# Kernel tuning notes

Hardware: AMD Instinct MI355X
Metric: run time of the kernel (lower is better)

## Reference

```python
import jax, jax.numpy as jnp
import numpy as np

INPUT_DIM = 512
HIDDEN_DIM = 512
SEQ_LEN = 512
BATCH = 128


def setup_inputs() -> dict:
    key = jax.random.key(0)
    ks = jax.random.split(key, 9)
    d_in = INPUT_DIM + HIDDEN_DIM
    s = 1.0 / np.sqrt(d_in)  # torch nn.Linear default init scale
    def lin(k):
        kw, kb = jax.random.split(k)
        W = jax.random.uniform(kw, (d_in, HIDDEN_DIM), jnp.float32, -s, s)
        b = jax.random.uniform(kb, (HIDDEN_DIM,), jnp.float32, -s, s)
        return W, b
    Wf, bf = lin(ks[0])
    Wi, bi = lin(ks[1])
    Wg, bg = lin(ks[2])
    Wo, bo = lin(ks[3])
    inputs = jax.random.normal(ks[4], (SEQ_LEN, BATCH, INPUT_DIM), jnp.float32)
    return {"inputs": inputs, "Wf": Wf, "bf": bf, "Wi": Wi, "bi": bi,
            "Wg": Wg, "bg": bg, "Wo": Wo, "bo": bo}


def reference(inputs, Wf, bf, Wi, bi, Wg, bg, Wo, bo):
    # Classical LSTM recurrence (n_qubits=0 path). inputs: [T, B, D_in]
    B = inputs.shape[1]
    hx = jnp.zeros((B, HIDDEN_DIM), inputs.dtype)
    cx = jnp.zeros((B, HIDDEN_DIM), inputs.dtype)
    # Stack the 4 gate weights so each step does one fused GEMM: [B, 1024] x [1024, 4H]
    W = jnp.concatenate([Wf, Wi, Wg, Wo], axis=1)  # [D_in+H, 4H]
    b = jnp.concatenate([bf, bi, bg, bo], axis=0)  # [4H]

    def step(carry, x):
        hx, cx = carry
        combined = jnp.concatenate([x, hx], axis=1)      # [B, D_in+H]
        gates = combined @ W + b                          # [B, 4H]
        f_, i_, g_, o_ = jnp.split(gates, 4, axis=1)
        f = jax.nn.sigmoid(f_)
        i = jax.nn.sigmoid(i_)
        g = jnp.tanh(g_)
        o = jax.nn.sigmoid(o_)
        cx = f * cx + i * g
        hx = o * jnp.tanh(cx)
        return (hx, cx), hx

    (hx, cx), outputs = jax.lax.scan(step, (hx, cx), inputs)
    return outputs, (hx, cx)
```

## Files before the change

kernel.cpp:

```cpp
#include <hip/hip_runtime.h>


typedef unsigned short u16;
typedef unsigned int   u32;
typedef unsigned long long u64;
typedef short bf16x8 __attribute__((ext_vector_type(8)));
typedef float f32x4  __attribute__((ext_vector_type(4)));

#define TT 512
#define BB 128
#define DD 512
#define HH 512
#define ASTRIDE 1032

__device__ __forceinline__ float bf2f(u16 u) { return __uint_as_float(((u32)u) << 16); }
__device__ __forceinline__ u16 f2bf(float f) {
    u32 u = __float_as_uint(f);
    return (u16)((u + 0x7FFFu + ((u >> 16) & 1u)) >> 16);
}
__device__ __forceinline__ u32 pack2(u16 a, u16 b) { return (u32)a | ((u32)b << 16); }
__device__ __forceinline__ float sigm(float x)  { return 1.0f / (1.0f + __expf(-x)); }
__device__ __forceinline__ float tanh_(float x) { return 1.0f - 2.0f / (1.0f + __expf(2.0f * x)); }

__launch_bounds__(256, 1)
__global__ void lstm_fused(const float* __restrict__ x,
                           const float* __restrict__ Wf, const float* __restrict__ bfv,
                           const float* __restrict__ Wi, const float* __restrict__ biv,
                           const float* __restrict__ Wg, const float* __restrict__ bgv,
                           const float* __restrict__ Wo, const float* __restrict__ bov,
                           float* __restrict__ out, u32* __restrict__ cnt,
                           u32* __restrict__ hbuf)
{
    __shared__ __align__(16) u16   aHi[16 * ASTRIDE];
    __shared__ __align__(16) u16   aLo[16 * ASTRIDE];
    __shared__ __align__(16) float xchg[4 * 4 * 16 * 20];

    const int tid  = threadIdx.x;
    const int lane = tid & 63;
    const int wv   = tid >> 6;
    const int l16  = lane & 15;
    const int quad = lane >> 4;
    const int blk  = blockIdx.x;
    const int mg   = blk & 7;
    const int nb   = blk >> 3;
    const int rowbase = mg * 16;
    const int kwb  = wv * 256;

    const float* Wq[4] = { Wf, Wi, Wg, Wo };
    bf16x8 whi[4][8], wlo[4][8];
#pragma unroll
    for (int q = 0; q < 4; ++q) {
        const float* Wp = Wq[q] + (size_t)(kwb + quad * 8) * HH + nb * 16 + l16;
#pragma unroll
        for (int s = 0; s < 8; ++s)
#pragma unroll
            for (int j = 0; j < 8; ++j) {
                float wval = Wp[(size_t)(s * 32 + j) * HH];
                u16 h = f2bf(wval);
                whi[q][s][j] = (short)h;
                wlo[q][s][j] = (short)f2bf(wval - bf2f(h));
            }
    }

    const int ec = tid & 15, er = tid >> 4;
    const int hcol = nb * 16 + ec;
    const float bias[4] = { bfv[hcol], biv[hcol], bgv[hcol], bov[hcol] };
    float cst = 0.0f;

    u32* myCnt = cnt + mg * 32;
    const int frow = tid >> 4;
    const int fch  = tid & 15;
    const u16* aHiB = aHi + l16 * ASTRIDE + kwb + quad * 8;
    const u16* aLoB = aLo + l16 * ASTRIDE + kwb + quad * 8;

    for (int t = 0; t < TT; ++t) {
        {
            u16* rowHi = aHi + frow * ASTRIDE;
            u16* rowLo = aLo + frow * ASTRIDE;
            const float4* xs = (const float4*)(x + ((size_t)t * BB + rowbase + frow) * DD + fch * 32);
#pragma unroll
            for (int g = 0; g < 4; ++g) {
                float4 a = xs[2 * g], b = xs[2 * g + 1];
                u16 h0 = f2bf(a.x), h1 = f2bf(a.y), h2 = f2bf(a.z), h3 = f2bf(a.w);
                u16 h4 = f2bf(b.x), h5 = f2bf(b.y), h6 = f2bf(b.z), h7 = f2bf(b.w);
                uint4 H = { pack2(h0, h1), pack2(h2, h3), pack2(h4, h5), pack2(h6, h7) };
                uint4 L = { pack2(f2bf(a.x - bf2f(h0)), f2bf(a.y - bf2f(h1))),
                            pack2(f2bf(a.z - bf2f(h2)), f2bf(a.w - bf2f(h3))),
                            pack2(f2bf(b.x - bf2f(h4)), f2bf(b.y - bf2f(h5))),
                            pack2(f2bf(b.z - bf2f(h6)), f2bf(b.w - bf2f(h7))) };
                ((uint4*)(rowHi + fch * 32))[g] = H;
                ((uint4*)(rowLo + fch * 32))[g] = L;
            }
            uint4* dH = (uint4*)(rowHi + 512 + fch * 32);
            uint4* dL = (uint4*)(rowLo + 512 + fch * 32);
            if (t == 0) {
                uint4 z = { 0u, 0u, 0u, 0u };
#pragma unroll
                for (int i = 0; i < 4; ++i) { dH[i] = z; dL[i] = z; }
            } else {
                const u64* hs = (const u64*)(hbuf + (size_t)((t - 1) & 1) * (BB * HH)
                                             + (size_t)(rowbase + frow) * HH + fch * 32);
                u32 hhp[16], hlp[16];
#pragma unroll
                for (int i = 0; i < 16; ++i) {
                    u64 v = __hip_atomic_load(hs + i, __ATOMIC_RELAXED, __HIP_MEMORY_SCOPE_AGENT);
                    u32 c0 = (u32)v, c1 = (u32)(v >> 32);
                    hhp[i] = (c0 & 0xFFFFu) | (c1 << 16);
                    hlp[i] = (c0 >> 16) | (c1 & 0xFFFF0000u);
                }
#pragma unroll
                for (int i = 0; i < 4; ++i) {
                    dH[i] = (uint4){ hhp[4*i], hhp[4*i+1], hhp[4*i+2], hhp[4*i+3] };
                    dL[i] = (uint4){ hlp[4*i], hlp[4*i+1], hlp[4*i+2], hlp[4*i+3] };
                }
            }
        }
        __syncthreads();

        f32x4 acc[4];
#pragma unroll
        for (int q = 0; q < 4; ++q) acc[q] = (f32x4){0.f, 0.f, 0.f, 0.f};
#pragma unroll
        for (int s = 0; s < 8; ++s) {
            bf16x8 ah = *(const bf16x8*)(aHiB + s * 32);
            bf16x8 al = *(const bf16x8*)(aLoB + s * 32);
#pragma unroll
            for (int q = 0; q < 4; ++q) {
                acc[q] = __builtin_amdgcn_mfma_f32_16x16x32_bf16(ah, whi[q][s], acc[q], 0, 0, 0);
                acc[q] = __builtin_amdgcn_mfma_f32_16x16x32_bf16(al, whi[q][s], acc[q], 0, 0, 0);
                acc[q] = __builtin_amdgcn_mfma_f32_16x16x32_bf16(ah, wlo[q][s], acc[q], 0, 0, 0);
            }
        }
#pragma unroll
        for (int q = 0; q < 4; ++q)
            *(f32x4*)&xchg[((wv * 4 + q) * 16 + l16) * 20 + quad * 4] = acc[q];
        __syncthreads();

        float pre[4];
#pragma unroll
        for (int q = 0; q < 4; ++q) {
            float p = bias[q];
#pragma unroll
            for (int ww = 0; ww < 4; ++ww) p += xchg[((ww * 4 + q) * 16 + ec) * 20 + er];
            pre[q] = p;
        }
        float fg = sigm(pre[0]);
        float ig = sigm(pre[1]);
        float gg = tanh_(pre[2]);
        float og = sigm(pre[3]);
        cst = fg * cst + ig * gg;
        float hv = og * tanh_(cst);

        const int gidx = (rowbase + er) * HH + hcol;
        out[(size_t)t * (BB * HH) + gidx] = hv;
        u16 hh = f2bf(hv);
        u16 hl = f2bf(hv - bf2f(hh));
        __hip_atomic_store(hbuf + (size_t)(t & 1) * (BB * HH) + gidx, pack2(hh, hl),
                           __ATOMIC_RELAXED, __HIP_MEMORY_SCOPE_AGENT);
        if (t == TT - 1) {
            out[(size_t)TT * (BB * HH) + gidx] = hv;
            out[(size_t)TT * (BB * HH) + BB * HH + gidx] = cst;
        }
        __syncthreads();

        if (tid == 0)
            __hip_atomic_fetch_add(myCnt, 1u, __ATOMIC_RELAXED, __HIP_MEMORY_SCOPE_AGENT);
        if (wv == 0) {
            const u32 tgt = 32u * (u32)(t + 1);
            while (__hip_atomic_load(myCnt, __ATOMIC_RELAXED, __HIP_MEMORY_SCOPE_AGENT) < tgt)
                __builtin_amdgcn_s_sleep(1);
        }
        __syncthreads();
    }
}

extern "C" void kernel_launch(void* const* d_in, const int* in_sizes, int n_in,
                              void* d_out, int out_size, void* d_ws, size_t ws_size,
                              hipStream_t stream) {
    (void)in_sizes; (void)n_in; (void)out_size; (void)ws_size;
    const float* x   = (const float*)d_in[0];
    const float* Wf  = (const float*)d_in[1];
    const float* bfv = (const float*)d_in[2];
    const float* Wi  = (const float*)d_in[3];
    const float* biv = (const float*)d_in[4];
    const float* Wg  = (const float*)d_in[5];
    const float* bgv = (const float*)d_in[6];
    const float* Wo  = (const float*)d_in[7];
    const float* bov = (const float*)d_in[8];

    u32* cnt  = (u32*)d_ws;
    u32* hbuf = (u32*)((char*)d_ws + 1024);

    hipMemsetAsync(d_ws, 0, 1024, stream);
    lstm_fused<<<dim3(256), dim3(256), 0, stream>>>(x, Wf, bfv, Wi, biv, Wg, bgv, Wo, bov,
                                                    (float*)d_out, cnt, hbuf);
}
```

Before: 4.855 ms.

## Replace counter barrier with step-tagged hidden-state polling and per-wave LDS slices

```diff
diff --git a/kernel.cpp b/kernel.cpp
--- a/kernel.cpp
+++ b/kernel.cpp
@@ -11,7 +11,6 @@
 #define BB 128
 #define DD 512
 #define HH 512
-#define ASTRIDE 1032
 
 __device__ __forceinline__ float bf2f(u16 u) { return __uint_as_float(((u32)u) << 16); }
 __device__ __forceinline__ u16 f2bf(float f) {
@@ -28,12 +27,10 @@
                            const float* __restrict__ Wi, const float* __restrict__ biv,
                            const float* __restrict__ Wg, const float* __restrict__ bgv,
                            const float* __restrict__ Wo, const float* __restrict__ bov,
-                           float* __restrict__ out, u32* __restrict__ cnt,
-                           u32* __restrict__ hbuf)
+                           float* __restrict__ out, u64* __restrict__ hbuf)
 {
-    __shared__ __align__(16) u16   aHi[16 * ASTRIDE];
-    __shared__ __align__(16) u16   aLo[16 * ASTRIDE];
-    __shared__ __align__(16) float xchg[4 * 4 * 16 * 20];
+    __shared__ __align__(16) u16   aPl[2 * 16 * 1024];
+    __shared__ __align__(16) float xch[2][4 * 4 * 16 * 20];
 
     const int tid  = threadIdx.x;
     const int lane = tid & 63;
@@ -45,6 +42,7 @@
     const int nb   = blk >> 3;
     const int rowbase = mg * 16;
     const int kwb  = wv * 256;
+    const bool isH = (wv >= 2);
 
     const float* Wq[4] = { Wf, Wi, Wg, Wo };
     bf16x8 whi[4][8], wlo[4][8];
@@ -66,20 +64,34 @@
     const int hcol = nb * 16 + ec;
     const float bias[4] = { bfv[hcol], biv[hcol], bgv[hcol], bov[hcol] };
     float cst = 0.0f;
-
-    u32* myCnt = cnt + mg * 32;
-    const int frow = tid >> 4;
-    const int fch  = tid & 15;
-    const u16* aHiB = aHi + l16 * ASTRIDE + kwb + quad * 8;
-    const u16* aLoB = aLo + l16 * ASTRIDE + kwb + quad * 8;
+    const int gidx = (rowbase + er) * HH + hcol;
+    u64* hout = hbuf + gidx;
+
+    const int srow = isH ? (lane & 15) : (lane >> 2);
+    const int scb  = isH ? (lane >> 4) : (lane & 3);
+
+    char* aB = (char*)aPl;
+    int wrA[8], rdA[8];
+    {
+        const int swzW = (srow & 7) << 4;
+#pragma unroll
+        for (int i = 0; i < 8; ++i)
+            wrA[i] = srow * 2048 + wv * 512 + ((scb * 128 + i * 16) ^ swzW);
+        const int swzR = (l16 & 7) << 4;
+#pragma unroll
+        for (int s = 0; s < 8; ++s)
+            rdA[s] = l16 * 2048 + wv * 512 + ((quad * 16 + s * 64) ^ swzR);
+    }
+
+    const float* xptr = x + (size_t)(rowbase + srow) * DD + kwb + scb * 64;
+    const u64*   hrow = hbuf + (size_t)(rowbase + srow) * HH
+                             + (isH ? (kwb - 512) : 0) + scb * 64;
 
     for (int t = 0; t < TT; ++t) {
-        {
-            u16* rowHi = aHi + frow * ASTRIDE;
-            u16* rowLo = aLo + frow * ASTRIDE;
-            const float4* xs = (const float4*)(x + ((size_t)t * BB + rowbase + frow) * DD + fch * 32);
-#pragma unroll
-            for (int g = 0; g < 4; ++g) {
+        if (!isH) {
+            const float4* xs = (const float4*)xptr;
+#pragma unroll
+            for (int g = 0; g < 8; ++g) {
                 float4 a = xs[2 * g], b = xs[2 * g + 1];
                 u16 h0 = f2bf(a.x), h1 = f2bf(a.y), h2 = f2bf(a.z), h3 = f2bf(a.w);
                 u16 h4 = f2bf(b.x), h5 = f2bf(b.y), h6 = f2bf(b.z), h7 = f2bf(b.w);
@@ -88,42 +100,51 @@
                             pack2(f2bf(a.z - bf2f(h2)), f2bf(a.w - bf2f(h3))),
                             pack2(f2bf(b.x - bf2f(h4)), f2bf(b.y - bf2f(h5))),
                             pack2(f2bf(b.z - bf2f(h6)), f2bf(b.w - bf2f(h7))) };
-                ((uint4*)(rowHi + fch * 32))[g] = H;
-                ((uint4*)(rowLo + fch * 32))[g] = L;
-            }
-            uint4* dH = (uint4*)(rowHi + 512 + fch * 32);
-            uint4* dL = (uint4*)(rowLo + 512 + fch * 32);
-            if (t == 0) {
-                uint4 z = { 0u, 0u, 0u, 0u };
-#pragma unroll
-                for (int i = 0; i < 4; ++i) { dH[i] = z; dL[i] = z; }
-            } else {
-                const u64* hs = (const u64*)(hbuf + (size_t)((t - 1) & 1) * (BB * HH)
-                                             + (size_t)(rowbase + frow) * HH + fch * 32);
-                u32 hhp[16], hlp[16];
-#pragma unroll
-                for (int i = 0; i < 16; ++i) {
-                    u64 v = __hip_atomic_load(hs + i, __ATOMIC_RELAXED, __HIP_MEMORY_SCOPE_AGENT);
-                    u32 c0 = (u32)v, c1 = (u32)(v >> 32);
-                    hhp[i] = (c0 & 0xFFFFu) | (c1 << 16);
-                    hlp[i] = (c0 >> 16) | (c1 & 0xFFFF0000u);
-                }
-#pragma unroll
-                for (int i = 0; i < 4; ++i) {
-                    dH[i] = (uint4){ hhp[4*i], hhp[4*i+1], hhp[4*i+2], hhp[4*i+3] };
-                    dL[i] = (uint4){ hlp[4*i], hlp[4*i+1], hlp[4*i+2], hlp[4*i+3] };
-                }
-            }
-        }
-        __syncthreads();
+                *(uint4*)(aB + wrA[g]) = H;
+                *(uint4*)(aB + wrA[g] + 32768) = L;
+            }
+            xptr += (size_t)BB * DD;
+        } else if (t == 0) {
+            uint4 z = { 0u, 0u, 0u, 0u };
+#pragma unroll
+            for (int g = 0; g < 8; ++g) {
+                *(uint4*)(aB + wrA[g]) = z;
+                *(uint4*)(aB + wrA[g] + 32768) = z;
+            }
+        } else {
+            const u64* hp = hrow + (size_t)((t - 1) & 1) * (BB * HH);
+            const u32 want = (u32)t;
+            u64 v[64];
+            for (;;) {
+#pragma unroll
+                for (int j = 0; j < 64; ++j)
+                    v[j] = __hip_atomic_load(hp + j, __ATOMIC_RELAXED, __HIP_MEMORY_SCOPE_AGENT);
+                u32 bad = 0;
+#pragma unroll
+                for (int j = 0; j < 64; ++j) bad |= ((u32)(v[j] >> 32)) ^ want;
+                if (bad == 0) break;
+            }
+#pragma unroll
+            for (int g = 0; g < 8; ++g) {
+                u32 p[8];
+#pragma unroll
+                for (int j = 0; j < 8; ++j) p[j] = (u32)v[g * 8 + j];
+                uint4 H = { (p[0] & 0xFFFFu) | (p[1] << 16), (p[2] & 0xFFFFu) | (p[3] << 16),
+                            (p[4] & 0xFFFFu) | (p[5] << 16), (p[6] & 0xFFFFu) | (p[7] << 16) };
+                uint4 L = { (p[0] >> 16) | (p[1] & 0xFFFF0000u), (p[2] >> 16) | (p[3] & 0xFFFF0000u),
+                            (p[4] >> 16) | (p[5] & 0xFFFF0000u), (p[6] >> 16) | (p[7] & 0xFFFF0000u) };
+                *(uint4*)(aB + wrA[g]) = H;
+                *(uint4*)(aB + wrA[g] + 32768) = L;
+            }
+        }
 
         f32x4 acc[4];
 #pragma unroll
         for (int q = 0; q < 4; ++q) acc[q] = (f32x4){0.f, 0.f, 0.f, 0.f};
 #pragma unroll
         for (int s = 0; s < 8; ++s) {
-            bf16x8 ah = *(const bf16x8*)(aHiB + s * 32);
-            bf16x8 al = *(const bf16x8*)(aLoB + s * 32);
+            bf16x8 ah = *(const bf16x8*)(aB + rdA[s]);
+            bf16x8 al = *(const bf16x8*)(aB + rdA[s] + 32768);
 #pragma unroll
             for (int q = 0; q < 4; ++q) {
                 acc[q] = __builtin_amdgcn_mfma_f32_16x16x32_bf16(ah, whi[q][s], acc[q], 0, 0, 0);
@@ -131,9 +152,10 @@
                 acc[q] = __builtin_amdgcn_mfma_f32_16x16x32_bf16(ah, wlo[q][s], acc[q], 0, 0, 0);
             }
         }
+        float* xc = xch[t & 1];
 #pragma unroll
         for (int q = 0; q < 4; ++q)
-            *(f32x4*)&xchg[((wv * 4 + q) * 16 + l16) * 20 + quad * 4] = acc[q];
+            *(f32x4*)&xc[((wv * 4 + q) * 16 + l16) * 20 + quad * 4] = acc[q];
         __syncthreads();
 
         float pre[4];
@@ -141,7 +163,7 @@
         for (int q = 0; q < 4; ++q) {
             float p = bias[q];
 #pragma unroll
-            for (int ww = 0; ww < 4; ++ww) p += xchg[((ww * 4 + q) * 16 + ec) * 20 + er];
+            for (int ww = 0; ww < 4; ++ww) p += xc[((ww * 4 + q) * 16 + ec) * 20 + er];
             pre[q] = p;
         }
         float fg = sigm(pre[0]);
@@ -151,26 +173,16 @@
         cst = fg * cst + ig * gg;
         float hv = og * tanh_(cst);
 
-        const int gidx = (rowbase + er) * HH + hcol;
-        out[(size_t)t * (BB * HH) + gidx] = hv;
         u16 hh = f2bf(hv);
         u16 hl = f2bf(hv - bf2f(hh));
-        __hip_atomic_store(hbuf + (size_t)(t & 1) * (BB * HH) + gidx, pack2(hh, hl),
+        __hip_atomic_store(hout + (size_t)(t & 1) * (BB * HH),
+                           ((u64)(u32)(t + 1) << 32) | (u64)pack2(hh, hl),
                            __ATOMIC_RELAXED, __HIP_MEMORY_SCOPE_AGENT);
+        out[(size_t)t * (BB * HH) + gidx] = hv;
         if (t == TT - 1) {
             out[(size_t)TT * (BB * HH) + gidx] = hv;
             out[(size_t)TT * (BB * HH) + BB * HH + gidx] = cst;
         }
-        __syncthreads();
-
-        if (tid == 0)
-            __hip_atomic_fetch_add(myCnt, 1u, __ATOMIC_RELAXED, __HIP_MEMORY_SCOPE_AGENT);
-        if (wv == 0) {
-            const u32 tgt = 32u * (u32)(t + 1);
-            while (__hip_atomic_load(myCnt, __ATOMIC_RELAXED, __HIP_MEMORY_SCOPE_AGENT) < tgt)
-                __builtin_amdgcn_s_sleep(1);
-        }
-        __syncthreads();
     }
 }
 
@@ -188,10 +200,9 @@
     const float* Wo  = (const float*)d_in[7];
     const float* bov = (const float*)d_in[8];
 
-    u32* cnt  = (u32*)d_ws;
-    u32* hbuf = (u32*)((char*)d_ws + 1024);
-
-    hipMemsetAsync(d_ws, 0, 1024, stream);
+    u64* hbuf = (u64*)d_ws;
+
+    hipMemsetAsync(d_ws, 0, (size_t)2 * BB * HH * 8, stream);
     lstm_fused<<<dim3(256), dim3(256), 0, stream>>>(x, Wf, bfv, Wi, biv, Wg, bgv, Wo, bov,
-                                                    (float*)d_out, cnt, hbuf);
+                                                    (float*)d_out, hbuf);
 }
```

After: 7.600 ms. 1.57x slower.
